# Kernel optimization log

Measured on AMD Instinct MI355X. Metric: run time of the kernel, lower is better.

The kernel has to match this reference:

```python
import jax, jax.numpy as jnp
import numpy as np


def _vec2ss(w):
    # 3x3 skew-symmetric matrix from a 3-vector
    zero = jnp.zeros((), dtype=w.dtype)
    return jnp.stack([
        jnp.stack([zero, -w[2], w[1]]),
        jnp.stack([w[2], zero, -w[0]]),
        jnp.stack([-w[1], w[0], zero]),
    ])


def _se3_exp(w, v, theta):
    K = _vec2ss(w)                      # 3x3 skew-symmetric
    KK = K @ K                          # 3x3
    I3 = jnp.eye(3, dtype=w.dtype)
    s, c = jnp.sin(theta), jnp.cos(theta)
    R = I3 + s * K + (1.0 - c) * KK                      # Rodrigues rotation
    V = I3 * theta + (1.0 - c) * K + (theta - s) * KK    # left Jacobian * theta
    t = V @ v                                            # translation (3,)
    top = jnp.concatenate([R, t[:, None]], axis=1)       # 3x4
    bottom = jnp.array([[0.0, 0.0, 0.0, 1.0]], dtype=w.dtype)
    return jnp.concatenate([top, bottom], axis=0)        # 4x4


def setup_inputs() -> dict:
    key = jax.random.key(0)
    k1, k2, k3, k4 = jax.random.split(key, 4)
    N = 16_000_000  # homogeneous points/columns to transform
    x = jax.random.normal(k1, (4, N), dtype=jnp.float32)
    w = jax.random.normal(k2, (3,), dtype=jnp.float32) * 1e-6
    v = jax.random.normal(k3, (3,), dtype=jnp.float32) * 1e-6
    theta = jax.random.normal(k4, (), dtype=jnp.float32) * 1e-6
    return {"x": x, "w": w, "v": v, "theta": theta}


def reference(x, w, v, theta):
    exp_i = _se3_exp(w, v, theta)   # 4x4 SE3 transform
    return exp_i @ x                # [4, N]
```

## Files before the change

kernel.cpp:

```cpp
#include <hip/hip_runtime.h>
#include <math.h>


typedef float f32x4 __attribute__((ext_vector_type(4)));

__global__ void se3_build_kernel(const float* __restrict__ w,
                                 const float* __restrict__ v,
                                 const float* __restrict__ th_p,
                                 float* __restrict__ M ) {
    if (threadIdx.x != 0 || blockIdx.x != 0) return;

    const float w0 = w[0], w1 = w[1], w2 = w[2];
    const float v0 = v[0], v1 = v[1], v2 = v[2];
    const float th = th_p[0];
    const float s = sinf(th);
    const float c = cosf(th);
    const float omc = 1.0f - c;
    const float tms = th - s;

    const float kk00 = -(w1 * w1 + w2 * w2);
    const float kk11 = -(w0 * w0 + w2 * w2);
    const float kk22 = -(w0 * w0 + w1 * w1);
    const float kk01 = w0 * w1;
    const float kk02 = w0 * w2;
    const float kk12 = w1 * w2;

    const float r00 = 1.0f + omc * kk00;
    const float r01 = -s * w2 + omc * kk01;
    const float r02 =  s * w1 + omc * kk02;
    const float r10 =  s * w2 + omc * kk01;
    const float r11 = 1.0f + omc * kk11;
    const float r12 = -s * w0 + omc * kk12;
    const float r20 = -s * w1 + omc * kk02;
    const float r21 =  s * w0 + omc * kk12;
    const float r22 = 1.0f + omc * kk22;

    const float V00 = th + tms * kk00;
    const float V01 = -omc * w2 + tms * kk01;
    const float V02 =  omc * w1 + tms * kk02;
    const float V10 =  omc * w2 + tms * kk01;
    const float V11 = th + tms * kk11;
    const float V12 = -omc * w0 + tms * kk12;
    const float V20 = -omc * w1 + tms * kk02;
    const float V21 =  omc * w0 + tms * kk12;
    const float V22 = th + tms * kk22;

    M[0]  = r00; M[1]  = r01; M[2]  = r02; M[3]  = V00 * v0 + V01 * v1 + V02 * v2;
    M[4]  = r10; M[5]  = r11; M[6]  = r12; M[7]  = V10 * v0 + V11 * v1 + V12 * v2;
    M[8]  = r20; M[9]  = r21; M[10] = r22; M[11] = V20 * v0 + V21 * v1 + V22 * v2;
}

__global__ __launch_bounds__(256) void se3_transform_kernel(
    const float* __restrict__ x,
    const float* __restrict__ M,
    float* __restrict__ out,
    int N)
{
    const float r00 = M[0], r01 = M[1], r02 = M[2],  t0 = M[3];
    const float r10 = M[4], r11 = M[5], r12 = M[6],  t1 = M[7];
    const float r20 = M[8], r21 = M[9], r22 = M[10], t2 = M[11];

    const int n4 = N >> 2;
    const int i4 = blockIdx.x * blockDim.x + threadIdx.x;

    if (i4 < n4) {
        const f32x4* x0p = (const f32x4*)(x);
        const f32x4* x1p = (const f32x4*)(x + (size_t)N);
        const f32x4* x2p = (const f32x4*)(x + 2 * (size_t)N);
        const f32x4* x3p = (const f32x4*)(x + 3 * (size_t)N);

        const f32x4 a = __builtin_nontemporal_load(x0p + i4);
        const f32x4 b = __builtin_nontemporal_load(x1p + i4);
        const f32x4 e = __builtin_nontemporal_load(x2p + i4);
        const f32x4 d = __builtin_nontemporal_load(x3p + i4);

        f32x4 o0, o1, o2;
        o0 = r00 * a + r01 * b + r02 * e + t0 * d;
        o1 = r10 * a + r11 * b + r12 * e + t1 * d;
        o2 = r20 * a + r21 * b + r22 * e + t2 * d;

        __builtin_nontemporal_store(o0, (f32x4*)(out) + i4);
        __builtin_nontemporal_store(o1, (f32x4*)(out + (size_t)N) + i4);
        __builtin_nontemporal_store(o2, (f32x4*)(out + 2 * (size_t)N) + i4);
        __builtin_nontemporal_store(d,  (f32x4*)(out + 3 * (size_t)N) + i4);
    }

    const int tail = N & 3;
    if (blockIdx.x == 0 && (int)threadIdx.x < tail) {
        const int j = (N & ~3) + (int)threadIdx.x;
        const float a = x[j];
        const float b = x[(size_t)N + j];
        const float e = x[2 * (size_t)N + j];
        const float d = x[3 * (size_t)N + j];
        out[j]                 = r00 * a + r01 * b + r02 * e + t0 * d;
        out[(size_t)N + j]     = r10 * a + r11 * b + r12 * e + t1 * d;
        out[2 * (size_t)N + j] = r20 * a + r21 * b + r22 * e + t2 * d;
        out[3 * (size_t)N + j] = d;
    }
}

extern "C" void kernel_launch(void* const* d_in, const int* in_sizes, int n_in,
                              void* d_out, int out_size, void* d_ws, size_t ws_size,
                              hipStream_t stream) {
    const float* x  = (const float*)d_in[0];
    const float* w  = (const float*)d_in[1];
    const float* v  = (const float*)d_in[2];
    const float* th = (const float*)d_in[3];
    float* out = (float*)d_out;
    float* M   = (float*)d_ws;

    const int N = in_sizes[0] / 4;
    const int n4 = N / 4;
    int blocks = (n4 + 255) / 256;
    if (blocks < 1) blocks = 1;

    se3_build_kernel<<<1, 64, 0, stream>>>(w, v, th, M);
    se3_transform_kernel<<<blocks, 256, 0, stream>>>(x, M, out, N);
}
```

Baseline: 409.2 us.

## Fuse SE3 matrix build into transform kernel and process two vectors per thread

```diff
diff --git a/kernel.cpp b/kernel.cpp
--- a/kernel.cpp
+++ b/kernel.cpp
@@ -4,14 +4,42 @@
 
 typedef float f32x4 __attribute__((ext_vector_type(4)));
 
-__global__ void se3_build_kernel(const float* __restrict__ w,
-                                 const float* __restrict__ v,
-                                 const float* __restrict__ th_p,
-                                 float* __restrict__ M ) {
-    if (threadIdx.x != 0 || blockIdx.x != 0) return;
+__global__ __launch_bounds__(256) void se3_fused_kernel(
+    const float* __restrict__ x,
+    const float* __restrict__ w,
+    const float* __restrict__ v,
+    const float* __restrict__ th_p,
+    float* __restrict__ out,
+    int N)
+{
+    const int n4 = N >> 2;
+    const int i0 = (int)blockIdx.x * ((int)blockDim.x * 2) + (int)threadIdx.x;
+    const int i1 = i0 + (int)blockDim.x;
+
+    const f32x4* x0p = (const f32x4*)(x);
+    const f32x4* x1p = (const f32x4*)(x + (size_t)N);
+    const f32x4* x2p = (const f32x4*)(x + 2 * (size_t)N);
+    const f32x4* x3p = (const f32x4*)(x + 3 * (size_t)N);
+
+    f32x4 a0 = {}, b0 = {}, e0 = {}, d0 = {};
+    f32x4 a1 = {}, b1 = {}, e1 = {}, d1 = {};
+    const bool p0 = (i0 < n4);
+    const bool p1 = (i1 < n4);
+    if (p0) {
+        a0 = __builtin_nontemporal_load(x0p + i0);
+        b0 = __builtin_nontemporal_load(x1p + i0);
+        e0 = __builtin_nontemporal_load(x2p + i0);
+        d0 = __builtin_nontemporal_load(x3p + i0);
+    }
+    if (p1) {
+        a1 = __builtin_nontemporal_load(x0p + i1);
+        b1 = __builtin_nontemporal_load(x1p + i1);
+        e1 = __builtin_nontemporal_load(x2p + i1);
+        d1 = __builtin_nontemporal_load(x3p + i1);
+    }
 
     const float w0 = w[0], w1 = w[1], w2 = w[2];
-    const float v0 = v[0], v1 = v[1], v2 = v[2];
+    const float vv0 = v[0], vv1 = v[1], vv2 = v[2];
     const float th = th_p[0];
     const float s = sinf(th);
     const float c = cosf(th);
@@ -45,44 +73,32 @@
     const float V21 =  omc * w0 + tms * kk12;
     const float V22 = th + tms * kk22;
 
-    M[0]  = r00; M[1]  = r01; M[2]  = r02; M[3]  = V00 * v0 + V01 * v1 + V02 * v2;
-    M[4]  = r10; M[5]  = r11; M[6]  = r12; M[7]  = V10 * v0 + V11 * v1 + V12 * v2;
-    M[8]  = r20; M[9]  = r21; M[10] = r22; M[11] = V20 * v0 + V21 * v1 + V22 * v2;
-}
+    const float t0 = V00 * vv0 + V01 * vv1 + V02 * vv2;
+    const float t1 = V10 * vv0 + V11 * vv1 + V12 * vv2;
+    const float t2 = V20 * vv0 + V21 * vv1 + V22 * vv2;
 
-__global__ __launch_bounds__(256) void se3_transform_kernel(
-    const float* __restrict__ x,
-    const float* __restrict__ M,
-    float* __restrict__ out,
-    int N)
-{
-    const float r00 = M[0], r01 = M[1], r02 = M[2],  t0 = M[3];
-    const float r10 = M[4], r11 = M[5], r12 = M[6],  t1 = M[7];
-    const float r20 = M[8], r21 = M[9], r22 = M[10], t2 = M[11];
+    f32x4* o0p = (f32x4*)(out);
+    f32x4* o1p = (f32x4*)(out + (size_t)N);
+    f32x4* o2p = (f32x4*)(out + 2 * (size_t)N);
+    f32x4* o3p = (f32x4*)(out + 3 * (size_t)N);
 
-    const int n4 = N >> 2;
-    const int i4 = blockIdx.x * blockDim.x + threadIdx.x;
-
-    if (i4 < n4) {
-        const f32x4* x0p = (const f32x4*)(x);
-        const f32x4* x1p = (const f32x4*)(x + (size_t)N);
-        const f32x4* x2p = (const f32x4*)(x + 2 * (size_t)N);
-        const f32x4* x3p = (const f32x4*)(x + 3 * (size_t)N);
-
-        const f32x4 a = __builtin_nontemporal_load(x0p + i4);
-        const f32x4 b = __builtin_nontemporal_load(x1p + i4);
-        const f32x4 e = __builtin_nontemporal_load(x2p + i4);
-        const f32x4 d = __builtin_nontemporal_load(x3p + i4);
-
-        f32x4 o0, o1, o2;
-        o0 = r00 * a + r01 * b + r02 * e + t0 * d;
-        o1 = r10 * a + r11 * b + r12 * e + t1 * d;
-        o2 = r20 * a + r21 * b + r22 * e + t2 * d;
-
-        __builtin_nontemporal_store(o0, (f32x4*)(out) + i4);
-        __builtin_nontemporal_store(o1, (f32x4*)(out + (size_t)N) + i4);
-        __builtin_nontemporal_store(o2, (f32x4*)(out + 2 * (size_t)N) + i4);
-        __builtin_nontemporal_store(d,  (f32x4*)(out + 3 * (size_t)N) + i4);
+    if (p0) {
+        const f32x4 y0 = r00 * a0 + r01 * b0 + r02 * e0 + t0 * d0;
+        const f32x4 y1 = r10 * a0 + r11 * b0 + r12 * e0 + t1 * d0;
+        const f32x4 y2 = r20 * a0 + r21 * b0 + r22 * e0 + t2 * d0;
+        __builtin_nontemporal_store(y0, o0p + i0);
+        __builtin_nontemporal_store(y1, o1p + i0);
+        __builtin_nontemporal_store(y2, o2p + i0);
+        __builtin_nontemporal_store(d0, o3p + i0);
+    }
+    if (p1) {
+        const f32x4 y0 = r00 * a1 + r01 * b1 + r02 * e1 + t0 * d1;
+        const f32x4 y1 = r10 * a1 + r11 * b1 + r12 * e1 + t1 * d1;
+        const f32x4 y2 = r20 * a1 + r21 * b1 + r22 * e1 + t2 * d1;
+        __builtin_nontemporal_store(y0, o0p + i1);
+        __builtin_nontemporal_store(y1, o1p + i1);
+        __builtin_nontemporal_store(y2, o2p + i1);
+        __builtin_nontemporal_store(d1, o3p + i1);
     }
 
     const int tail = N & 3;
@@ -107,13 +123,13 @@
     const float* v  = (const float*)d_in[2];
     const float* th = (const float*)d_in[3];
     float* out = (float*)d_out;
-    float* M   = (float*)d_ws;
+    (void)d_ws; (void)ws_size;
 
     const int N = in_sizes[0] / 4;
     const int n4 = N / 4;
-    int blocks = (n4 + 255) / 256;
+    const int per_block = 256 * 2;
+    int blocks = (n4 + per_block - 1) / per_block;
     if (blocks < 1) blocks = 1;
 
-    se3_build_kernel<<<1, 64, 0, stream>>>(w, v, th, M);
-    se3_transform_kernel<<<blocks, 256, 0, stream>>>(x, M, out, N);
+    se3_fused_kernel<<<blocks, 256, 0, stream>>>(x, w, v, th, out, N);
 }
```

New measurement: 406.5 us. Within noise of the previous version (-0.6%).
